# Kernel optimization log

Measured on AMD Instinct MI355X. Metric: run time of the kernel, lower is better.

## Reference

```python
import jax, jax.numpy as jnp
import numpy as np

B, S, T = 128, 2048, 128


def setup_inputs() -> dict:
    key = jax.random.key(0)
    k1, k2, k3, k4, k5, k6 = jax.random.split(key, 6)
    logit = jax.random.normal(k1, (B, S, T), jnp.float32)
    target = jax.random.randint(k2, (B, S), 0, T, dtype=jnp.int32)
    seq_lens = jax.random.randint(k3, (B,), 1, S + 1, dtype=jnp.int32)
    transitions = 0.1 * jax.random.normal(k4, (T, T), jnp.float32)
    start_transitions = 0.1 * jax.random.normal(k5, (T,), jnp.float32)
    end_transitions = 0.1 * jax.random.normal(k6, (T,), jnp.float32)
    return dict(logit=logit, target=target, seq_lens=seq_lens,
                transitions=transitions, start_transitions=start_transitions,
                end_transitions=end_transitions)


def reference(logit, target, seq_lens, transitions, start_transitions, end_transitions):
    # logit: [B,S,T] batch-first; CRF works time-first like the torch code's transpose(0,1)
    em = jnp.transpose(logit, (1, 0, 2))          # [S,B,T]
    tg = target.T                                  # [S,B]
    mask = jnp.arange(S)[:, None] < seq_lens[None, :]  # [S,B]

    # ---- loss: -mean log-likelihood (CRF forward algorithm) ----
    emit = jnp.take_along_axis(em, tg[..., None], -1)[..., 0]   # [S,B]
    trans_sc = transitions[tg[:-1], tg[1:]]                      # [S-1,B]
    num = start_transitions[tg[0]] + emit[0]
    num = num + jnp.sum(jnp.where(mask[1:], emit[1:] + trans_sc, 0.0), axis=0)
    last_tags = jnp.take_along_axis(tg, (seq_lens - 1)[None, :], 0)[0]  # [B]
    num = num + end_transitions[last_tags]

    def fstep(alpha, xs):
        e_t, m_t = xs  # [B,T], [B]
        nxt = jax.nn.logsumexp(alpha[:, :, None] + transitions[None] + e_t[:, None, :], axis=1)
        return jnp.where(m_t[:, None], nxt, alpha), None

    alpha0 = start_transitions[None, :] + em[0]   # [B,T]
    alpha, _ = jax.lax.scan(fstep, alpha0, (em[1:], mask[1:]))
    logZ = jax.nn.logsumexp(alpha + end_transitions[None, :], axis=-1)  # [B]
    loss = -(num - logZ).mean()

    # ---- Viterbi decode ----
    tag_ids = jnp.arange(T, dtype=jnp.int32)

    def vstep(score, xs):
        e_t, m_t = xs
        mat = score[:, :, None] + transitions[None] + e_t[:, None, :]  # [B,Tprev,Tcur]
        best = mat.max(axis=1)
        idx = mat.argmax(axis=1).astype(jnp.int32)
        score = jnp.where(m_t[:, None], best, score)
        idx = jnp.where(m_t[:, None], idx, tag_ids[None, :])  # identity beyond seq end
        return score, idx

    vscore, hist = jax.lax.scan(vstep, alpha0, (em[1:], mask[1:]))  # hist: [S-1,B,T]
    last_tag = jnp.argmax(vscore + end_transitions[None, :], axis=-1).astype(jnp.int32)

    def bstep(tag, idx_t):
        prev = jnp.take_along_axis(idx_t, tag[:, None], 1)[:, 0]
        return prev, prev

    _, tags_prev = jax.lax.scan(bstep, last_tag, hist, reverse=True)  # [S-1,B]
    pred = jnp.concatenate([tags_prev, last_tag[None, :]], axis=0).T  # [B,S]

    # ---- _rearrange_output: swap decoded-tag logit with the max logit ----
    maxidx = jnp.argmax(logit, axis=-1)                         # [B,S]
    maxval = jnp.max(logit, axis=-1)                            # [B,S]
    vval = jnp.take_along_axis(logit, pred[..., None], -1)[..., 0]  # [B,S]
    oh_v = pred[..., None] == tag_ids[None, None, :]
    oh_m = maxidx[..., None] == tag_ids[None, None, :]
    swapped = jnp.where(oh_v, maxval[..., None],
                        jnp.where(oh_m, vval[..., None], logit))
    log_probs = jax.nn.log_softmax(swapped, axis=-1)            # [B,S,T]

    return loss, pred, log_probs
```

## Files before the change

kernel.cpp:

```cpp
#include <hip/hip_runtime.h>
#include <stdint.h>

#define BB 128
#define SS 2048
#define TT 128
#define NSEG 32
#define SEGK 64

typedef float f32x4 __attribute__((ext_vector_type(4)));

#define BAR() asm volatile("s_waitcnt lgkmcnt(0)\n\ts_barrier" ::: "memory")

#define PIN(x) asm volatile("" : "+v"(x))

__attribute__((amdgpu_flat_work_group_size(256, 256)))
__attribute__((amdgpu_waves_per_eu(1, 1)))
__global__ void crf_mainX(const float* __restrict__ logit,
                          const int* __restrict__ seq_lens,
                          const float* __restrict__ trans,
                          const float* __restrict__ startT,
                          const float* __restrict__ endT,
                          const int* __restrict__ target,
                          uint8_t* __restrict__ histG,
                          float* __restrict__ scr_logZ,
                          int* __restrict__ scr_last,
                          float* __restrict__ scr_num)
{
    extern __shared__ float smem[];
    float* transLDS = smem;
    float* vecLDS   = smem + 16384;
    float* ringLDS  = smem + 16384 + 256;
    float* redLDS   = smem + 16384 + 260;
    int*   redILDS  = (int*)(smem + 16384 + 268);
    float* sumLDS   = smem + 16384 + 272;

    const int bid = blockIdx.x;
    const int role = bid >> 7;
    const int b = bid & (BB - 1);
    const int tid = threadIdx.x;
    const int j = tid >> 1;
    const int h = tid & 1;
    const int ibase0 = h << 6;
    const int L = seq_lens[b];
    const size_t lbase = (size_t)b * (SS * TT);

    {
        const float4* g = (const float4*)trans;
        float4* l = (float4*)transLDS;
        for (int k = tid; k < (TT * TT) / 4; k += 256) l[k] = g[k];
    }
    __syncthreads();

    float e1 = 0.f, e2 = 0.f;
    if (L > 1) e1 = logit[lbase + TT + j];
    e2 = (L > 2) ? logit[lbase + 2 * (size_t)TT + j] : e1;

    if (role == 0) {
        f32x4 tC[16];
#pragma unroll
        for (int c = 0; c < 16; ++c) {
            tC[c].x = transLDS[(ibase0 + c * 4 + 0) * TT + j];
            tC[c].y = transLDS[(ibase0 + c * 4 + 1) * TT + j];
            tC[c].z = transLDS[(ibase0 + c * 4 + 2) * TT + j];
            tC[c].w = transLDS[(ibase0 + c * 4 + 3) * TT + j];
            PIN(tC[c]);
        }
        const float a0 = startT[j] + logit[lbase + j];
        if (h == 0) vecLDS[j] = a0;
        __syncthreads();

        for (int t = 1; t < L; ++t) {
            const int cur = (t - 1) & 1, nxt = t & 1;
            const float e = e1; e1 = e2;
            const int tn = (t + 2 < L) ? (t + 2) : (L - 1);
            e2 = logit[lbase + (size_t)tn * TT + j];

            const f32x4* sq = (const f32x4*)(vecLDS + cur * TT + ibase0);
            float cm[8];
#pragma unroll
            for (int c = 0; c < 8; ++c) {
                f32x4 sa = sq[2 * c], sb = sq[2 * c + 1];
                f32x4 ta = tC[2 * c], tb = tC[2 * c + 1];
                float p0 = sa.x + ta.x, p1 = sa.y + ta.y;
                float p2 = sa.z + ta.z, p3 = sa.w + ta.w;
                float p4 = sb.x + tb.x, p5 = sb.y + tb.y;
                float p6 = sb.z + tb.z, p7 = sb.w + tb.w;
                float A  = fmaxf(fmaxf(p0, p1), p2);
                float Bm = fmaxf(fmaxf(p3, p4), p5);
                float C  = fmaxf(p6, p7);
                cm[c] = fmaxf(fmaxf(A, Bm), C);
            }
            float M = fmaxf(fmaxf(fmaxf(cm[0], cm[1]), cm[2]),
                            fmaxf(fmaxf(cm[3], cm[4]),
                                  fmaxf(cm[5], fmaxf(cm[6], cm[7]))));
            const float Mo = __shfl_xor(M, 1);
            const float Mall = fmaxf(M, Mo);
            const float v = Mall + e;

            int cwin = -1;
#pragma unroll
            for (int c = 7; c >= 0; --c) cwin = ((cm[c] + e) == v) ? c : cwin;

            int idx = 0x7fffffff;
            if (cwin >= 0) {
                const int basei = ibase0 + cwin * 8;
                const float* tr = transLDS + (size_t)basei * TT + j;
                const f32x4* sr = (const f32x4*)(vecLDS + cur * TT + basei);
                f32x4 ra = sr[0], rb = sr[1];
                float q0 = (ra.x + tr[0 * TT]) + e;
                float q1 = (ra.y + tr[1 * TT]) + e;
                float q2 = (ra.z + tr[2 * TT]) + e;
                float q3 = (ra.w + tr[3 * TT]) + e;
                float q4 = (rb.x + tr[4 * TT]) + e;
                float q5 = (rb.y + tr[5 * TT]) + e;
                float q6 = (rb.z + tr[6 * TT]) + e;
                float q7 = (rb.w + tr[7 * TT]) + e;
                idx = (q7 == v) ? basei + 7 : idx;
                idx = (q6 == v) ? basei + 6 : idx;
                idx = (q5 == v) ? basei + 5 : idx;
                idx = (q4 == v) ? basei + 4 : idx;
                idx = (q3 == v) ? basei + 3 : idx;
                idx = (q2 == v) ? basei + 2 : idx;
                idx = (q1 == v) ? basei + 1 : idx;
                idx = (q0 == v) ? basei + 0 : idx;
            }
            const int oidx = __shfl_xor(idx, 1);
            idx = (oidx < idx) ? oidx : idx;

            if (h == 0) {
                vecLDS[nxt * TT + j] = v;
                histG[(size_t)b * (SS * TT) + (size_t)t * TT + j] = (uint8_t)idx;
            }
            BAR();
        }

        const int fin = (L - 1) & 1;
        if (tid < 128) {
            float lv = vecLDS[fin * TT + tid] + endT[tid];
            int li = tid;
#pragma unroll
            for (int off = 1; off < 64; off <<= 1) {
                float ov = __shfl_xor(lv, off);
                int oi = __shfl_xor(li, off);
                if (ov > lv || (ov == lv && oi < li)) { lv = ov; li = oi; }
            }
            if ((tid & 63) == 0) { redLDS[tid >> 6] = lv; redILDS[tid >> 6] = li; }
        }
        __syncthreads();
        if (tid == 0) {
            int lt = (redLDS[1] > redLDS[0] ||
                      (redLDS[1] == redLDS[0] && redILDS[1] < redILDS[0]))
                     ? redILDS[1] : redILDS[0];
            scr_last[b] = lt;
        }
        uint8_t* hb = histG + (size_t)b * (SS * TT);
        const int colq = (tid & 7) * 16;
        const uint32_t w0 = 0x03020100u + 0x01010101u * (uint32_t)colq;
        const uint4 pat = make_uint4(w0, w0 + 0x04040404u, w0 + 0x08080808u, w0 + 0x0C0C0C0Cu);
        for (int t0 = L; t0 < SS; t0 += 32) {
            int t = t0 + (tid >> 3);
            if (t < SS) *(uint4*)(hb + (size_t)t * TT + colq) = pat;
        }
    } else {
        f32x4 tE[16];
#pragma unroll
        for (int c = 0; c < 16; ++c) {
            tE[c].x = __expf(transLDS[(ibase0 + c * 4 + 0) * TT + j]);
            tE[c].y = __expf(transLDS[(ibase0 + c * 4 + 1) * TT + j]);
            tE[c].z = __expf(transLDS[(ibase0 + c * 4 + 2) * TT + j]);
            tE[c].w = __expf(transLDS[(ibase0 + c * 4 + 3) * TT + j]);
            PIN(tE[c]);
        }
        const float a0 = startT[j] + logit[lbase + j];
        const float R0 = startT[0] + logit[lbase + 0];
        float alpha = a0;
        if (h == 0) vecLDS[j] = __expf(a0 - R0);
        if (tid < 4) ringLDS[tid] = R0;
        __syncthreads();

        for (int t = 1; t < L; ++t) {
            const int cur = (t - 1) & 1, nxt = t & 1;
            const float Rcons = ringLDS[(t - 3) & 3];
            const float Rpub  = ringLDS[(t - 2) & 3];
            const float e = e1; e1 = e2;
            const int tn = (t + 2 < L) ? (t + 2) : (L - 1);
            e2 = logit[lbase + (size_t)tn * TT + j];

            const f32x4* aq = (const f32x4*)(vecLDS + cur * TT + ibase0);
            float s0 = 0.f, s1 = 0.f, s2 = 0.f, s3 = 0.f;
#pragma unroll
            for (int c = 0; c < 16; ++c) {
                f32x4 av = aq[c]; f32x4 tv = tE[c];
                s0 = fmaf(av.x, tv.x, s0);
                s1 = fmaf(av.y, tv.y, s1);
                s2 = fmaf(av.z, tv.z, s2);
                s3 = fmaf(av.w, tv.w, s3);
            }
            float Ssum = (s0 + s1) + (s2 + s3);
            Ssum += __shfl_xor(Ssum, 1);
            alpha = e + Rcons + __logf(Ssum);
            const float p = __expf(alpha - Rpub);
            if (h == 0) vecLDS[nxt * TT + j] = p;
            if (tid == 0) ringLDS[t & 3] = alpha;
            BAR();
        }

        const float fval = alpha + endT[j];
        float tmx = fval;
#pragma unroll
        for (int off = 1; off < 64; off <<= 1) tmx = fmaxf(tmx, __shfl_xor(tmx, off));
        if ((tid & 63) == 0) redLDS[4 + (tid >> 6)] = tmx;
        __syncthreads();
        const float gm = fmaxf(fmaxf(redLDS[4], redLDS[5]), fmaxf(redLDS[6], redLDS[7]));
        float se = (h == 0) ? __expf(fval - gm) : 0.f;
#pragma unroll
        for (int off = 1; off < 64; off <<= 1) se += __shfl_xor(se, off);
        if ((tid & 63) == 0) sumLDS[tid >> 6] = se;
        __syncthreads();
        if (tid == 0)
            scr_logZ[b] = gm + __logf(sumLDS[0] + sumLDS[1] + sumLDS[2] + sumLDS[3]);
        __syncthreads();

        float acc = 0.f;
        for (int t = tid; t < L; t += 256) {
            int tg = target[b * SS + t];
            acc += logit[((size_t)b * SS + t) * TT + tg];
            if (t >= 1) acc += trans[target[b * SS + t - 1] * TT + tg];
        }
#pragma unroll
        for (int off = 1; off < 64; off <<= 1) acc += __shfl_xor(acc, off);
        if ((tid & 63) == 0) sumLDS[tid >> 6] = acc;
        __syncthreads();
        if (tid == 0) {
            float tot = sumLDS[0] + sumLDS[1] + sumLDS[2] + sumLDS[3];
            tot += startT[target[b * SS]] + endT[target[b * SS + L - 1]];
            scr_num[b] = tot;
        }
    }
}

__global__ void crf_btseg(uint8_t* __restrict__ histG)
{
    const int c = blockIdx.x;
    const int b = blockIdx.y;
    const int tid = threadIdx.x;
    __shared__ __align__(16) uint8_t hl[SEGK * TT];

    const int lo = (c == 0) ? 1 : c * SEGK;
    const int nr = (c == 0) ? 63 : 64;
    const uint8_t* src = histG + (size_t)b * (SS * TT) + (size_t)lo * TT;
    for (int k = tid; k < (nr * TT) / 16; k += 128)
        ((uint4*)hl)[k] = ((const uint4*)src)[k];
    __syncthreads();

    int tau = tid;
    uint32_t w[16];
#pragma unroll
    for (int q = 0; q < 16; ++q) w[q] = 0u;
    if (c == 0) {
#pragma unroll
        for (int r = 62; r >= 0; --r) {
            tau = hl[r * TT + tau];
            w[r >> 2] |= ((uint32_t)tau) << ((r & 3) * 8);
        }
    } else {
#pragma unroll
        for (int r = 63; r >= 0; --r) {
            tau = hl[r * TT + tau];
            w[r >> 2] |= ((uint32_t)tau) << ((r & 3) * 8);
        }
    }
    uint4* dst = (uint4*)(histG + (size_t)b * (SS * TT) + (size_t)c * 8192 + (size_t)tid * 64);
    dst[0] = make_uint4(w[0], w[1], w[2], w[3]);
    dst[1] = make_uint4(w[4], w[5], w[6], w[7]);
    dst[2] = make_uint4(w[8], w[9], w[10], w[11]);
    dst[3] = make_uint4(w[12], w[13], w[14], w[15]);
}

__global__ void crf_btchain(const uint8_t* __restrict__ histG,
                            const int* __restrict__ scr_last,
                            int* __restrict__ scr_bt,
                            float* __restrict__ out_pred)
{
    const int b = threadIdx.x;
    if (b >= BB) return;
    int tau = scr_last[b];
    out_pred[(size_t)b * SS + (SS - 1)] = (float)tau;
    for (int c = NSEG - 1; c >= 0; --c) {
        scr_bt[b * NSEG + c] = tau;
        tau = histG[(size_t)b * (SS * TT) + (size_t)c * 8192 + (size_t)tau * 64];
    }
}

__global__ void crf_btfill(const uint8_t* __restrict__ histG,
                           const int* __restrict__ scr_bt,
                           float* __restrict__ out_pred)
{
    const int c = blockIdx.x;
    const int b = blockIdx.y;
    const int s = threadIdx.x;
    if (c == 0 && s > 62) return;
    const int js = scr_bt[b * NSEG + c];
    uint8_t v = histG[(size_t)b * (SS * TT) + (size_t)c * 8192 + (size_t)js * 64 + s];
    const int pos = (c == 0) ? s : (c * SEGK - 1 + s);
    out_pred[(size_t)b * SS + pos] = (float)v;
}

__global__ void crf_loss(const float* __restrict__ scr_logZ, const float* __restrict__ scr_num,
                         float* __restrict__ out)
{
    const int tid = threadIdx.x;
    __shared__ float p2[2];
    float v = (tid < BB) ? (scr_logZ[tid] - scr_num[tid]) : 0.0f;
#pragma unroll
    for (int off = 1; off < 64; off <<= 1) v += __shfl_xor(v, off);
    if ((tid & 63) == 0) p2[tid >> 6] = v;
    __syncthreads();
    if (tid == 0) out[0] = (p2[0] + p2[1]) / (float)BB;
}

__global__ void crf_logprobs(const float* __restrict__ logit,
                             const float* __restrict__ predF,
                             float* __restrict__ outLP)
{
    const int wid = threadIdx.x >> 6;
    const int lane = threadIdx.x & 63;
    const size_t row = (size_t)blockIdx.x * 4 + wid;
    const float2* rp = (const float2*)(logit + row * TT);
    float2 v = rp[lane];
    const int pred = (int)predF[row];

    float mv; int mi;
    if (v.y > v.x) { mv = v.y; mi = lane * 2 + 1; }
    else           { mv = v.x; mi = lane * 2; }
#pragma unroll
    for (int off = 1; off < 64; off <<= 1) {
        float ov = __shfl_xor(mv, off);
        int oi = __shfl_xor(mi, off);
        if (ov > mv || (ov == mv && oi < mi)) { mv = ov; mi = oi; }
    }
    float se = __expf(v.x - mv) + __expf(v.y - mv);
#pragma unroll
    for (int off = 1; off < 64; off <<= 1) se += __shfl_xor(se, off);
    const float lse = __logf(se);

    float px = __shfl(v.x, pred >> 1);
    float py = __shfl(v.y, pred >> 1);
    float vp = (pred & 1) ? py : px;

    float ox = (lane * 2 == pred) ? mv : ((lane * 2 == mi) ? vp : v.x);
    float oy = (lane * 2 + 1 == pred) ? mv : ((lane * 2 + 1 == mi) ? vp : v.y);
    float* op = outLP + row * TT + lane * 2;
    op[0] = (ox - mv) - lse;
    op[1] = (oy - mv) - lse;
}

extern "C" void kernel_launch(void* const* d_in, const int* in_sizes, int n_in,
                              void* d_out, int out_size, void* d_ws, size_t ws_size,
                              hipStream_t stream)
{
    const float* logit    = (const float*)d_in[0];
    const int*   target   = (const int*)d_in[1];
    const int*   seq_lens = (const int*)d_in[2];
    const float* trans    = (const float*)d_in[3];
    const float* startT   = (const float*)d_in[4];
    const float* endT     = (const float*)d_in[5];

    float* out      = (float*)d_out;
    float* out_pred = out + 1;
    float* outLP    = out + 1 + (size_t)BB * SS;
    uint8_t* histG  = (uint8_t*)(out + 262148);
    float* scr      = out + ((size_t)1 + (size_t)BB * SS + (size_t)BB * SS * TT - 4480);
    float* scr_logZ = scr;
    float* scr_num  = scr + 128;
    int*   scr_last = (int*)(scr + 256);
    int*   scr_bt   = (int*)(scr + 384);

    const int dynLDS = (16384 + 288) * 4;
    hipFuncSetAttribute((const void*)crf_mainX,
                        hipFuncAttributeMaxDynamicSharedMemorySize, dynLDS);

    crf_mainX<<<2 * BB, 256, dynLDS, stream>>>(logit, seq_lens, trans, startT, endT,
                                               target, histG, scr_logZ, scr_last, scr_num);
    crf_btseg<<<dim3(NSEG, BB), 128, 0, stream>>>(histG);
    crf_btchain<<<1, 128, 0, stream>>>(histG, scr_last, scr_bt, out_pred);
    crf_btfill<<<dim3(NSEG, BB), 64, 0, stream>>>(histG, scr_bt, out_pred);
    crf_loss<<<1, 128, 0, stream>>>(scr_logZ, scr_num, out);
    crf_logprobs<<<(BB * SS) / 4, 256, 0, stream>>>(logit, out_pred, outLP);
}
```

Measured before the change: 1.767 ms.

## Pad LDS layouts, use DPP lane swaps, deepen emission prefetch in CRF recurrences

Pads the transitions matrix in LDS to a row stride of 129 and splits the alpha/score vector into two halves offset by 68 floats, so the two half-lanes reading different vector halves avoid LDS bank conflicts. Replaces the __shfl_xor pair exchanges with DPP quad-permute swaps, avoiding ds_bpermute round trips on the serial critical path. Extends emission prefetching from two steps ahead to three, and rewrites the max and dot-product inner loops in vector form with a flatter reduction tree. The cost is slightly more LDS, an uncoalesced scalar transitions load at startup, and one more live register.

```diff
diff --git a/kernel.cpp b/kernel.cpp
--- a/kernel.cpp
+++ b/kernel.cpp
@@ -7,11 +7,24 @@
 #define NSEG 32
 #define SEGK 64
 
+#define TRP 129
+#define VSTRIDE 136
+#define H1OFF 68
+
 typedef float f32x4 __attribute__((ext_vector_type(4)));
 
 #define BAR() asm volatile("s_waitcnt lgkmcnt(0)\n\ts_barrier" ::: "memory")
 
 #define PIN(x) asm volatile("" : "+v"(x))
+
+__device__ __forceinline__ float dpp_swap1_f(float x) {
+    int i = __float_as_int(x);
+    i = __builtin_amdgcn_update_dpp(0, i, 0xB1, 0xF, 0xF, true);
+    return __int_as_float(i);
+}
+__device__ __forceinline__ int dpp_swap1_i(int x) {
+    return __builtin_amdgcn_update_dpp(0, x, 0xB1, 0xF, 0xF, true);
+}
 
 __attribute__((amdgpu_flat_work_group_size(256, 256)))
 __attribute__((amdgpu_waves_per_eu(1, 1)))
@@ -28,11 +41,11 @@
 {
     extern __shared__ float smem[];
     float* transLDS = smem;
-    float* vecLDS   = smem + 16384;
-    float* ringLDS  = smem + 16384 + 256;
-    float* redLDS   = smem + 16384 + 260;
-    int*   redILDS  = (int*)(smem + 16384 + 268);
-    float* sumLDS   = smem + 16384 + 272;
+    float* vecLDS   = smem + 16512;
+    float* ringLDS  = smem + 16512 + 272;
+    float* redLDS   = smem + 16512 + 276;
+    int*   redILDS  = (int*)(smem + 16512 + 284);
+    float* sumLDS   = smem + 16512 + 288;
 
     const int bid = blockIdx.x;
     const int role = bid >> 7;
@@ -41,60 +54,52 @@
     const int j = tid >> 1;
     const int h = tid & 1;
     const int ibase0 = h << 6;
+    const int joff = j + ((j >= 64) ? (H1OFF - 64) : 0);
     const int L = seq_lens[b];
     const size_t lbase = (size_t)b * (SS * TT);
 
-    {
-        const float4* g = (const float4*)trans;
-        float4* l = (float4*)transLDS;
-        for (int k = tid; k < (TT * TT) / 4; k += 256) l[k] = g[k];
-    }
+    for (int m = tid; m < TT * TT; m += 256)
+        transLDS[(m >> 7) * TRP + (m & 127)] = trans[m];
     __syncthreads();
 
-    float e1 = 0.f, e2 = 0.f;
+    float e1 = 0.f, e2 = 0.f, e3 = 0.f;
     if (L > 1) e1 = logit[lbase + TT + j];
     e2 = (L > 2) ? logit[lbase + 2 * (size_t)TT + j] : e1;
+    e3 = (L > 3) ? logit[lbase + 3 * (size_t)TT + j] : e2;
 
     if (role == 0) {
         f32x4 tC[16];
 #pragma unroll
         for (int c = 0; c < 16; ++c) {
-            tC[c].x = transLDS[(ibase0 + c * 4 + 0) * TT + j];
-            tC[c].y = transLDS[(ibase0 + c * 4 + 1) * TT + j];
-            tC[c].z = transLDS[(ibase0 + c * 4 + 2) * TT + j];
-            tC[c].w = transLDS[(ibase0 + c * 4 + 3) * TT + j];
+            tC[c].x = transLDS[(ibase0 + c * 4 + 0) * TRP + j];
+            tC[c].y = transLDS[(ibase0 + c * 4 + 1) * TRP + j];
+            tC[c].z = transLDS[(ibase0 + c * 4 + 2) * TRP + j];
+            tC[c].w = transLDS[(ibase0 + c * 4 + 3) * TRP + j];
             PIN(tC[c]);
         }
         const float a0 = startT[j] + logit[lbase + j];
-        if (h == 0) vecLDS[j] = a0;
+        if (h == 0) vecLDS[joff] = a0;
         __syncthreads();
 
         for (int t = 1; t < L; ++t) {
             const int cur = (t - 1) & 1, nxt = t & 1;
-            const float e = e1; e1 = e2;
-            const int tn = (t + 2 < L) ? (t + 2) : (L - 1);
-            e2 = logit[lbase + (size_t)tn * TT + j];
-
-            const f32x4* sq = (const f32x4*)(vecLDS + cur * TT + ibase0);
+            const float e = e1; e1 = e2; e2 = e3;
+            const int tn = (t + 3 < L) ? (t + 3) : (L - 1);
+            e3 = logit[lbase + (size_t)tn * TT + j];
+
+            const f32x4* sq = (const f32x4*)(vecLDS + cur * VSTRIDE + h * H1OFF);
             float cm[8];
 #pragma unroll
             for (int c = 0; c < 8; ++c) {
-                f32x4 sa = sq[2 * c], sb = sq[2 * c + 1];
-                f32x4 ta = tC[2 * c], tb = tC[2 * c + 1];
-                float p0 = sa.x + ta.x, p1 = sa.y + ta.y;
-                float p2 = sa.z + ta.z, p3 = sa.w + ta.w;
-                float p4 = sb.x + tb.x, p5 = sb.y + tb.y;
-                float p6 = sb.z + tb.z, p7 = sb.w + tb.w;
-                float A  = fmaxf(fmaxf(p0, p1), p2);
-                float Bm = fmaxf(fmaxf(p3, p4), p5);
-                float C  = fmaxf(p6, p7);
-                cm[c] = fmaxf(fmaxf(A, Bm), C);
-            }
-            float M = fmaxf(fmaxf(fmaxf(cm[0], cm[1]), cm[2]),
-                            fmaxf(fmaxf(cm[3], cm[4]),
-                                  fmaxf(cm[5], fmaxf(cm[6], cm[7]))));
-            const float Mo = __shfl_xor(M, 1);
-            const float Mall = fmaxf(M, Mo);
+                f32x4 pa = sq[2 * c] + tC[2 * c];
+                f32x4 pb = sq[2 * c + 1] + tC[2 * c + 1];
+                float m01 = fmaxf(pa.x, pa.y), m23 = fmaxf(pa.z, pa.w);
+                float m45 = fmaxf(pb.x, pb.y), m67 = fmaxf(pb.z, pb.w);
+                cm[c] = fmaxf(fmaxf(m01, m23), fmaxf(m45, m67));
+            }
+            float M = fmaxf(fmaxf(fmaxf(cm[0], cm[1]), fmaxf(cm[2], cm[3])),
+                            fmaxf(fmaxf(cm[4], cm[5]), fmaxf(cm[6], cm[7])));
+            const float Mall = fmaxf(M, dpp_swap1_f(M));
             const float v = Mall + e;
 
             int cwin = -1;
@@ -104,17 +109,17 @@
             int idx = 0x7fffffff;
             if (cwin >= 0) {
                 const int basei = ibase0 + cwin * 8;
-                const float* tr = transLDS + (size_t)basei * TT + j;
-                const f32x4* sr = (const f32x4*)(vecLDS + cur * TT + basei);
+                const float* tr = transLDS + (size_t)basei * TRP + j;
+                const f32x4* sr = (const f32x4*)(vecLDS + cur * VSTRIDE + h * H1OFF + cwin * 8);
                 f32x4 ra = sr[0], rb = sr[1];
-                float q0 = (ra.x + tr[0 * TT]) + e;
-                float q1 = (ra.y + tr[1 * TT]) + e;
-                float q2 = (ra.z + tr[2 * TT]) + e;
-                float q3 = (ra.w + tr[3 * TT]) + e;
-                float q4 = (rb.x + tr[4 * TT]) + e;
-                float q5 = (rb.y + tr[5 * TT]) + e;
-                float q6 = (rb.z + tr[6 * TT]) + e;
-                float q7 = (rb.w + tr[7 * TT]) + e;
+                float q0 = (ra.x + tr[0 * TRP]) + e;
+                float q1 = (ra.y + tr[1 * TRP]) + e;
+                float q2 = (ra.z + tr[2 * TRP]) + e;
+                float q3 = (ra.w + tr[3 * TRP]) + e;
+                float q4 = (rb.x + tr[4 * TRP]) + e;
+                float q5 = (rb.y + tr[5 * TRP]) + e;
+                float q6 = (rb.z + tr[6 * TRP]) + e;
+                float q7 = (rb.w + tr[7 * TRP]) + e;
                 idx = (q7 == v) ? basei + 7 : idx;
                 idx = (q6 == v) ? basei + 6 : idx;
                 idx = (q5 == v) ? basei + 5 : idx;
@@ -124,11 +129,11 @@
                 idx = (q1 == v) ? basei + 1 : idx;
                 idx = (q0 == v) ? basei + 0 : idx;
             }
-            const int oidx = __shfl_xor(idx, 1);
+            const int oidx = dpp_swap1_i(idx);
             idx = (oidx < idx) ? oidx : idx;
 
             if (h == 0) {
-                vecLDS[nxt * TT + j] = v;
+                vecLDS[nxt * VSTRIDE + joff] = v;
                 histG[(size_t)b * (SS * TT) + (size_t)t * TT + j] = (uint8_t)idx;
             }
             BAR();
@@ -136,7 +141,8 @@
 
         const int fin = (L - 1) & 1;
         if (tid < 128) {
-            float lv = vecLDS[fin * TT + tid] + endT[tid];
+            const int toff = tid + ((tid >= 64) ? (H1OFF - 64) : 0);
+            float lv = vecLDS[fin * VSTRIDE + toff] + endT[tid];
             int li = tid;
 #pragma unroll
             for (int off = 1; off < 64; off <<= 1) {
@@ -165,16 +171,16 @@
         f32x4 tE[16];
 #pragma unroll
         for (int c = 0; c < 16; ++c) {
-            tE[c].x = __expf(transLDS[(ibase0 + c * 4 + 0) * TT + j]);
-            tE[c].y = __expf(transLDS[(ibase0 + c * 4 + 1) * TT + j]);
-            tE[c].z = __expf(transLDS[(ibase0 + c * 4 + 2) * TT + j]);
-            tE[c].w = __expf(transLDS[(ibase0 + c * 4 + 3) * TT + j]);
+            tE[c].x = __expf(transLDS[(ibase0 + c * 4 + 0) * TRP + j]);
+            tE[c].y = __expf(transLDS[(ibase0 + c * 4 + 1) * TRP + j]);
+            tE[c].z = __expf(transLDS[(ibase0 + c * 4 + 2) * TRP + j]);
+            tE[c].w = __expf(transLDS[(ibase0 + c * 4 + 3) * TRP + j]);
             PIN(tE[c]);
         }
         const float a0 = startT[j] + logit[lbase + j];
         const float R0 = startT[0] + logit[lbase + 0];
         float alpha = a0;
-        if (h == 0) vecLDS[j] = __expf(a0 - R0);
+        if (h == 0) vecLDS[joff] = __expf(a0 - R0);
         if (tid < 4) ringLDS[tid] = R0;
         __syncthreads();
 
@@ -182,25 +188,24 @@
             const int cur = (t - 1) & 1, nxt = t & 1;
             const float Rcons = ringLDS[(t - 3) & 3];
             const float Rpub  = ringLDS[(t - 2) & 3];
-            const float e = e1; e1 = e2;
-            const int tn = (t + 2 < L) ? (t + 2) : (L - 1);
-            e2 = logit[lbase + (size_t)tn * TT + j];
-
-            const f32x4* aq = (const f32x4*)(vecLDS + cur * TT + ibase0);
-            float s0 = 0.f, s1 = 0.f, s2 = 0.f, s3 = 0.f;
-#pragma unroll
-            for (int c = 0; c < 16; ++c) {
-                f32x4 av = aq[c]; f32x4 tv = tE[c];
-                s0 = fmaf(av.x, tv.x, s0);
-                s1 = fmaf(av.y, tv.y, s1);
-                s2 = fmaf(av.z, tv.z, s2);
-                s3 = fmaf(av.w, tv.w, s3);
-            }
-            float Ssum = (s0 + s1) + (s2 + s3);
-            Ssum += __shfl_xor(Ssum, 1);
+            const float e = e1; e1 = e2; e2 = e3;
+            const int tn = (t + 3 < L) ? (t + 3) : (L - 1);
+            e3 = logit[lbase + (size_t)tn * TT + j];
+
+            const f32x4* aq = (const f32x4*)(vecLDS + cur * VSTRIDE + h * H1OFF);
+            f32x4 s4 = {0.f, 0.f, 0.f, 0.f};
+            f32x4 s4b = {0.f, 0.f, 0.f, 0.f};
+#pragma unroll
+            for (int c = 0; c < 16; c += 2) {
+                s4  = aq[c] * tE[c] + s4;
+                s4b = aq[c + 1] * tE[c + 1] + s4b;
+            }
+            f32x4 st = s4 + s4b;
+            float Ssum = (st.x + st.y) + (st.z + st.w);
+            Ssum += dpp_swap1_f(Ssum);
             alpha = e + Rcons + __logf(Ssum);
             const float p = __expf(alpha - Rpub);
-            if (h == 0) vecLDS[nxt * TT + j] = p;
+            if (h == 0) vecLDS[nxt * VSTRIDE + joff] = p;
             if (tid == 0) ringLDS[t & 3] = alpha;
             BAR();
         }
@@ -376,7 +381,7 @@
     int*   scr_last = (int*)(scr + 256);
     int*   scr_bt   = (int*)(scr + 384);
 
-    const int dynLDS = (16384 + 288) * 4;
+    const int dynLDS = (16512 + 272 + 4 + 8 + 4 + 4 + 8) * 4;
     hipFuncSetAttribute((const void*)crf_mainX,
                         hipFuncAttributeMaxDynamicSharedMemorySize, dynLDS);
 
```

After: 1.591 ms. 1.11x faster.
